# Kernel optimization log

Measured on AMD Instinct MI355X. Metric: run time of the kernel, lower is better.

## Reference

```python
import jax, jax.numpy as jnp
import numpy as np

DIM, D_STATE, D_CONV = 1024, 16, 4
B, T = 2, 4096


def setup_inputs() -> dict:
    key = jax.random.key(0)
    ks = jax.random.split(key, 10)
    s = 0.02
    x = jax.random.normal(ks[0], (B, T, DIM), dtype=jnp.float32)
    W_in = jax.random.normal(ks[1], (DIM, 2 * DIM), dtype=jnp.float32) * s
    conv_w = jax.random.normal(ks[2], (DIM, D_CONV), dtype=jnp.float32) * s
    conv_b = jnp.zeros((DIM,), dtype=jnp.float32)
    A_log = jnp.log(jnp.tile(jnp.arange(1, D_STATE + 1, dtype=jnp.float32), (DIM, 1)))
    D_param = jnp.ones((DIM,), dtype=jnp.float32)
    W_x = jax.random.normal(ks[3], (DIM, 2 * D_STATE), dtype=jnp.float32) * s
    W_dt = jax.random.normal(ks[4], (DIM, DIM), dtype=jnp.float32) * s
    b_dt = jnp.zeros((DIM,), dtype=jnp.float32)
    W_out = jax.random.normal(ks[5], (DIM, DIM), dtype=jnp.float32) * s
    return {"x": x, "W_in": W_in, "conv_w": conv_w, "conv_b": conv_b,
            "A_log": A_log, "D_param": D_param, "W_x": W_x,
            "W_dt": W_dt, "b_dt": b_dt, "W_out": W_out}


def _mamba_fwd(x, W_in, conv_w, conv_b, A_log, D_param, W_x, W_dt, b_dt, W_out):
    Bsz, Tlen, D = x.shape
    N = A_log.shape[1]
    # input projection and gate split
    xz = jnp.einsum('btd,de->bte', x, W_in)          # [B,T,2D]
    x_in, z = jnp.split(xz, 2, axis=-1)
    # causal depthwise conv1d (torch pads both sides d_conv-1 then slices [:T] == left-pad only)
    xc = jnp.transpose(x_in, (0, 2, 1))               # [B,D,T]
    kern = conv_w[:, None, :]                         # [D,1,K] (O,I/groups,K)
    xc = jax.lax.conv_general_dilated(
        xc, kern, window_strides=(1,), padding=[(D_CONV - 1, 0)],
        dimension_numbers=('NCH', 'OIH', 'NCH'), feature_group_count=D)
    xc = xc + conv_b[None, :, None]
    x_in = jnp.transpose(xc, (0, 2, 1))               # [B,T,D]
    x_in = jax.nn.silu(x_in)
    # SSM parameters
    A = -jnp.exp(A_log)                               # [D,N]
    BC = jnp.einsum('btd,dn->btn', x_in, W_x)         # [B,T,2N]
    Bm, Cm = jnp.split(BC, 2, axis=-1)                # each [B,T,N]
    dt = jax.nn.softplus(jnp.einsum('btd,de->bte', x_in, W_dt) + b_dt)  # [B,T,D]
    # selective scan over time
    def step(h, inputs):
        dt_t, B_t, C_t, x_t = inputs                  # [B,D],[B,N],[B,N],[B,D]
        A_eff = jnp.exp(dt_t[:, :, None] * A[None])   # [B,D,N]
        B_eff = dt_t[:, :, None] * B_t[:, None, :]    # [B,D,N]
        h = A_eff * h + B_eff * x_t[:, :, None]
        y_t = jnp.sum(h * C_t[:, None, :], axis=-1) + D_param * x_t
        return h, y_t
    h0 = jnp.zeros((Bsz, D, N), dtype=x.dtype)
    xs = (jnp.transpose(dt, (1, 0, 2)), jnp.transpose(Bm, (1, 0, 2)),
          jnp.transpose(Cm, (1, 0, 2)), jnp.transpose(x_in, (1, 0, 2)))
    _, ys = jax.lax.scan(step, h0, xs)                # ys: [T,B,D]
    y = jnp.transpose(ys, (1, 0, 2))                  # [B,T,D]
    y = y * jax.nn.silu(z)
    return jnp.einsum('btd,de->bte', y, W_out)


def reference(x, W_in, conv_w, conv_b, A_log, D_param, W_x, W_dt, b_dt, W_out):
    return _mamba_fwd(x, W_in, conv_w, conv_b, A_log, D_param, W_x, W_dt, b_dt, W_out)
```

## Files before the change

### kernel.cpp

```cpp
#include <hip/hip_runtime.h>
#include <math.h>

#define DIM 1024
#define DSTATE 16
#define DCONV 4
#define BATCH 2
#define TLEN 4096
#define NC 128
#define LC (TLEN / NC)

typedef short s16x8 __attribute__((ext_vector_type(8)));
typedef float f32x4 __attribute__((ext_vector_type(4)));

__device__ __forceinline__ unsigned short f32_to_bf16(float f) {
    unsigned int u = __float_as_uint(f);
    u += 0x7fffu + ((u >> 16) & 1u);
    return (unsigned short)(u >> 16);
}
__device__ __forceinline__ float bf16_to_f32(unsigned short s) {
    return __uint_as_float(((unsigned int)s) << 16);
}

__device__ __forceinline__ void async16(const void* g, void* l) {
    __builtin_amdgcn_global_load_lds(
        (const __attribute__((address_space(1))) void*)g,
        (__attribute__((address_space(3))) void*)l, 16, 0, 0);
}

__device__ __forceinline__ size_t ps_addr(size_t i) {
    return ((i >> 10) << 11) | (i & 1023);
}

template <int EPI>
__global__ __launch_bounds__(256) void gemm_bf16s(
    const unsigned short* __restrict__ Ah, const unsigned short* __restrict__ Al,
    const unsigned short* __restrict__ Bh, const unsigned short* __restrict__ Bl,
    const float* __restrict__ bias, float* __restrict__ C,
    float* __restrict__ C2, int M, int N, int K)
{
    __shared__ unsigned short sAh[128][32];
    __shared__ unsigned short sAl[128][32];
    __shared__ unsigned short sBh[128][32];
    __shared__ unsigned short sBl[128][32];

    const int tid  = threadIdx.x;
    const int lane = tid & 63;
    const int w    = tid >> 6;
    const int wm   = (w >> 1) * 64;
    const int wn   = (w & 1) * 64;
    const int m0   = blockIdx.y * 128;
    const int n0   = blockIdx.x * 128;

    f32x4 acc[4][4];
#pragma unroll
    for (int i = 0; i < 4; ++i)
#pragma unroll
        for (int j = 0; j < 4; ++j) acc[i][j] = (f32x4){0.f, 0.f, 0.f, 0.f};

    const int srow  = w * 16 + (lane >> 2);
    const int skoff = (((lane & 3) ^ ((lane >> 3) & 3)) * 8);
    const size_t aRow0 = (size_t)(m0 + srow) * K;
    const size_t aRow1 = (size_t)(m0 + srow + 64) * K;
    const size_t bRow0 = (size_t)(n0 + srow) * K;
    const size_t bRow1 = (size_t)(n0 + srow + 64) * K;

    const int frow = lane & 15;
    const int fqd  = (((lane >> 4) ^ ((lane >> 1) & 3)) * 8);

    for (int k0 = 0; k0 < K; k0 += 32) {
        __syncthreads();
        async16(&Ah[aRow0 + k0 + skoff], &sAh[w * 16][0]);
        async16(&Ah[aRow1 + k0 + skoff], &sAh[64 + w * 16][0]);
        async16(&Al[aRow0 + k0 + skoff], &sAl[w * 16][0]);
        async16(&Al[aRow1 + k0 + skoff], &sAl[64 + w * 16][0]);
        async16(&Bh[bRow0 + k0 + skoff], &sBh[w * 16][0]);
        async16(&Bh[bRow1 + k0 + skoff], &sBh[64 + w * 16][0]);
        async16(&Bl[bRow0 + k0 + skoff], &sBl[w * 16][0]);
        async16(&Bl[bRow1 + k0 + skoff], &sBl[64 + w * 16][0]);
        __syncthreads();

        s16x8 fah[4], fal[4], fbh[4], fbl[4];
#pragma unroll
        for (int i = 0; i < 4; ++i) {
            fah[i] = *(const s16x8*)&sAh[wm + i * 16 + frow][fqd];
            fal[i] = *(const s16x8*)&sAl[wm + i * 16 + frow][fqd];
            fbh[i] = *(const s16x8*)&sBh[wn + i * 16 + frow][fqd];
            fbl[i] = *(const s16x8*)&sBl[wn + i * 16 + frow][fqd];
        }
#pragma unroll
        for (int mi = 0; mi < 4; ++mi)
#pragma unroll
            for (int ni = 0; ni < 4; ++ni) {
                acc[mi][ni] = __builtin_amdgcn_mfma_f32_16x16x32_bf16(
                    fah[mi], fbh[ni], acc[mi][ni], 0, 0, 0);
                acc[mi][ni] = __builtin_amdgcn_mfma_f32_16x16x32_bf16(
                    fah[mi], fbl[ni], acc[mi][ni], 0, 0, 0);
                acc[mi][ni] = __builtin_amdgcn_mfma_f32_16x16x32_bf16(
                    fal[mi], fbh[ni], acc[mi][ni], 0, 0, 0);
            }
    }

    const int erow = (lane >> 4) * 4;
    const int ecol = lane & 15;
#pragma unroll
    for (int mi = 0; mi < 4; ++mi)
#pragma unroll
        for (int ni = 0; ni < 4; ++ni) {
            const int colbase = n0 + wn + ni * 16;
            if (EPI == 2 && colbase >= 1024 + 2 * DSTATE) continue;
            const int col = colbase + ecol;
            if (EPI == 2 && colbase >= 1024) {
#pragma unroll
                for (int r = 0; r < 4; ++r) {
                    const int row = m0 + wm + mi * 16 + erow + r;
                    C2[(size_t)row * (2 * DSTATE) + (col - 1024)] = acc[mi][ni][r];
                }
            } else {
                const float bv = (EPI >= 1) ? bias[col] : 0.f;
                const int ldc = (EPI == 2) ? DIM : N;
#pragma unroll
                for (int r = 0; r < 4; ++r) {
                    const int row = m0 + wm + mi * 16 + erow + r;
                    float v = acc[mi][ni][r];
                    if (EPI >= 1) {
                        v += bv;
                        v = (v > 20.f) ? v : log1pf(__expf(v));
                    }
                    C[(size_t)row * ldc + col] = v;
                }
            }
        }
}

__global__ __launch_bounds__(256) void split_kernel(
    const float* __restrict__ src, unsigned short* __restrict__ h,
    unsigned short* __restrict__ l)
{
    size_t i = (size_t)blockIdx.x * 256 + threadIdx.x;
    float v = src[i];
    unsigned short hv = f32_to_bf16(v);
    h[i] = hv;
    l[i] = f32_to_bf16(v - bf16_to_f32(hv));
}

__global__ __launch_bounds__(256) void split_transpose_kernel(
    const float* __restrict__ W, unsigned short* __restrict__ Th,
    unsigned short* __restrict__ Tl, int Kdim, int Ndim)
{
    __shared__ float tile[32][33];
    const int n0 = blockIdx.x * 32;
    const int k0 = blockIdx.y * 32;
    const int tx = threadIdx.x & 31;
    const int ty = threadIdx.x >> 5;
    for (int r = ty; r < 32; r += 8)
        tile[r][tx] = W[(size_t)(k0 + r) * Ndim + n0 + tx];
    __syncthreads();
    for (int r = ty; r < 32; r += 8) {
        float v = tile[tx][r];
        unsigned short hv = f32_to_bf16(v);
        size_t o = (size_t)(n0 + r) * Kdim + k0 + tx;
        Th[o] = hv;
        Tl[o] = f32_to_bf16(v - bf16_to_f32(hv));
    }
}

__global__ __launch_bounds__(256) void conv_silu_kernel(
    const float* __restrict__ xz, const float* __restrict__ conv_w,
    const float* __restrict__ conv_b, float* __restrict__ x_in,
    unsigned short* __restrict__ xh, unsigned short* __restrict__ xl)
{
    size_t idx = (size_t)blockIdx.x * 256 + threadIdx.x;
    int d = (int)(idx & (DIM - 1));
    size_t bt = idx >> 10;
    int t = (int)(bt & (TLEN - 1));

    float acc = conv_b[d];
#pragma unroll
    for (int k = 0; k < DCONV; ++k) {
        int tt = t - (DCONV - 1) + k;
        if (tt >= 0) {
            acc = fmaf(xz[(bt - (DCONV - 1) + k) * (2 * DIM) + d],
                       conv_w[d * DCONV + k], acc);
        }
    }
    float s = acc / (1.f + __expf(-acc));
    x_in[idx] = s;
    unsigned short hv = f32_to_bf16(s);
    xh[idx] = hv;
    xl[idx] = f32_to_bf16(s - bf16_to_f32(hv));
}

__global__ __launch_bounds__(256) void scan_pass_a(
    const float* __restrict__ dt, const float* __restrict__ BC,
    const float* __restrict__ x_in, const float* __restrict__ A_log,
    float* __restrict__ Pb, float* __restrict__ Sb)
{
    __shared__ float sB[LC][DSTATE];
    const int tid = threadIdx.x;
    int blk = blockIdx.x;
    const int dt4 = blk & 3;  blk >>= 2;
    const int c = blk & (NC - 1); blk >>= 7;
    const int b = blk;
    const int d = dt4 * 256 + tid;
    const size_t base = (size_t)b * TLEN + (size_t)c * LC;

    if (tid < LC * DSTATE / 4) {
        const int row = tid >> 2, c4 = tid & 3;
        *(f32x4*)&sB[row][c4 * 4] =
            *(const f32x4*)&BC[(base + row) * (2 * DSTATE) + c4 * 4];
    }

    float A[DSTATE];
#pragma unroll
    for (int q = 0; q < 4; ++q) {
        f32x4 v = *(const f32x4*)&A_log[(size_t)d * DSTATE + q * 4];
        A[q * 4 + 0] = -__expf(v.x); A[q * 4 + 1] = -__expf(v.y);
        A[q * 4 + 2] = -__expf(v.z); A[q * 4 + 3] = -__expf(v.w);
    }
    __syncthreads();

    float h[DSTATE];
#pragma unroll
    for (int n = 0; n < DSTATE; ++n) h[n] = 0.f;
    float sdt = 0.f;

    for (int t = 0; t < LC; ++t) {
        const float dtv = dt[(base + t) * DIM + d];
        const float xv  = x_in[(base + t) * DIM + d];
        sdt += dtv;
        const float dbx = dtv * xv;
#pragma unroll
        for (int n = 0; n < DSTATE; ++n) {
            const float a = __expf(dtv * A[n]);
            h[n] = fmaf(a, h[n], dbx * sB[t][n]);
        }
    }

    const size_t po = ps_addr((((size_t)c * BATCH + b) * DIM + d) * DSTATE);
#pragma unroll
    for (int q = 0; q < 4; ++q) {
        f32x4 pv;
        pv.x = __expf(A[q * 4 + 0] * sdt);
        pv.y = __expf(A[q * 4 + 1] * sdt);
        pv.z = __expf(A[q * 4 + 2] * sdt);
        pv.w = __expf(A[q * 4 + 3] * sdt);
        *(f32x4*)&Pb[po + q * 4] = pv;
        *(f32x4*)&Sb[po + q * 4] = *(f32x4*)&h[q * 4];
    }
}

__global__ __launch_bounds__(256) void scan_pass_b(
    float* __restrict__ Pb, const float* __restrict__ Sb)
{
    const size_t idx = (size_t)blockIdx.x * 256 + threadIdx.x;
    float h = 0.f;
#pragma unroll 4
    for (int c = 0; c < NC; ++c) {
        const size_t o = (size_t)c * (BATCH * DIM * DSTATE) + idx;
        const size_t a = ps_addr(o);
        const float p = Pb[a];
        const float s = Sb[a];
        Pb[a] = h;
        h = fmaf(p, h, s);
    }
}

__global__ __launch_bounds__(256) void scan_pass_c(
    const float* __restrict__ dt, const float* __restrict__ BC,
    const float* __restrict__ xz, const float* __restrict__ A_log,
    const float* __restrict__ D_param, const float* __restrict__ Hin,
    const float* __restrict__ x_in,
    unsigned short* __restrict__ yh, unsigned short* __restrict__ yl)
{
    __shared__ float sB[LC][DSTATE];
    __shared__ float sC[LC][DSTATE];
    const int tid = threadIdx.x;
    int blk = blockIdx.x;
    const int dt4 = blk & 3;  blk >>= 2;
    const int c = blk & (NC - 1); blk >>= 7;
    const int b = blk;
    const int d = dt4 * 256 + tid;
    const size_t base = (size_t)b * TLEN + (size_t)c * LC;

    if (tid < 128) {
        const int row = tid >> 2, c4 = tid & 3;
        *(f32x4*)&sB[row][c4 * 4] =
            *(const f32x4*)&BC[(base + row) * (2 * DSTATE) + c4 * 4];
    } else {
        const int sj = tid - 128;
        const int row = sj >> 2, c4 = sj & 3;
        *(f32x4*)&sC[row][c4 * 4] =
            *(const f32x4*)&BC[(base + row) * (2 * DSTATE) + DSTATE + c4 * 4];
    }

    float A[DSTATE];
#pragma unroll
    for (int q = 0; q < 4; ++q) {
        f32x4 v = *(const f32x4*)&A_log[(size_t)d * DSTATE + q * 4];
        A[q * 4 + 0] = -__expf(v.x); A[q * 4 + 1] = -__expf(v.y);
        A[q * 4 + 2] = -__expf(v.z); A[q * 4 + 3] = -__expf(v.w);
    }
    const float Dp = D_param[d];

    float h[DSTATE];
    const size_t po = ps_addr((((size_t)c * BATCH + b) * DIM + d) * DSTATE);
#pragma unroll
    for (int q = 0; q < 4; ++q)
        *(f32x4*)&h[q * 4] = *(const f32x4*)&Hin[po + q * 4];
    __syncthreads();

    for (int t = 0; t < LC; ++t) {
        const float dtv = dt[(base + t) * DIM + d];
        const float xv  = x_in[(base + t) * DIM + d];
        const float zv  = xz[(base + t) * (2 * DIM) + DIM + d];
        const float dbx = dtv * xv;
        float y0 = 0.f, y1 = 0.f, y2 = 0.f, y3 = 0.f;
#pragma unroll
        for (int q = 0; q < 4; ++q) {
            float a0 = __expf(dtv * A[q * 4 + 0]);
            float a1 = __expf(dtv * A[q * 4 + 1]);
            float a2 = __expf(dtv * A[q * 4 + 2]);
            float a3 = __expf(dtv * A[q * 4 + 3]);
            h[q * 4 + 0] = fmaf(a0, h[q * 4 + 0], dbx * sB[t][q * 4 + 0]);
            h[q * 4 + 1] = fmaf(a1, h[q * 4 + 1], dbx * sB[t][q * 4 + 1]);
            h[q * 4 + 2] = fmaf(a2, h[q * 4 + 2], dbx * sB[t][q * 4 + 2]);
            h[q * 4 + 3] = fmaf(a3, h[q * 4 + 3], dbx * sB[t][q * 4 + 3]);
            y0 = fmaf(h[q * 4 + 0], sC[t][q * 4 + 0], y0);
            y1 = fmaf(h[q * 4 + 1], sC[t][q * 4 + 1], y1);
            y2 = fmaf(h[q * 4 + 2], sC[t][q * 4 + 2], y2);
            y3 = fmaf(h[q * 4 + 3], sC[t][q * 4 + 3], y3);
        }
        float y = (y0 + y1) + (y2 + y3) + Dp * xv;
        const float sig = 1.f / (1.f + __expf(-zv));
        const float yg = y * (zv * sig);
        unsigned short hv = f32_to_bf16(yg);
        yh[(base + t) * DIM + d] = hv;
        yl[(base + t) * DIM + d] = f32_to_bf16(yg - bf16_to_f32(hv));
    }
}

extern "C" void kernel_launch(void* const* d_in, const int* in_sizes, int n_in,
                              void* d_out, int out_size, void* d_ws, size_t ws_size,
                              hipStream_t stream)
{
    const float* x      = (const float*)d_in[0];
    const float* W_in   = (const float*)d_in[1];
    const float* conv_w = (const float*)d_in[2];
    const float* conv_b = (const float*)d_in[3];
    const float* A_log  = (const float*)d_in[4];
    const float* D_par  = (const float*)d_in[5];
    const float* W_x    = (const float*)d_in[6];
    const float* W_dt   = (const float*)d_in[7];
    const float* b_dt   = (const float*)d_in[8];
    const float* W_out  = (const float*)d_in[9];
    float* out = (float*)d_out;

    const size_t BT = (size_t)BATCH * TLEN;
    float* ws = (float*)d_ws;
    float* xz   = ws;
    float* x_in = xz + BT * (2 * DIM);
    float* dtb  = x_in + BT * DIM;
    float* BCb  = dtb + BT * DIM;

    unsigned short* bfAh = (unsigned short*)(BCb + BT * 2 * DSTATE);
    unsigned short* bfAl = bfAh + BT * DIM;
    unsigned short* WinTh = bfAl + BT * DIM;
    unsigned short* WinTl = WinTh + (size_t)2048 * 1024;
    unsigned short* W2Th  = WinTl + (size_t)2048 * 1024;
    unsigned short* W2Tl  = W2Th + (size_t)1152 * 1024;
    unsigned short* WoutTh = W2Tl + (size_t)1152 * 1024;
    unsigned short* WoutTl = WoutTh + (size_t)1024 * 1024;

    float* Pb = xz;
    float* Sb = xz + (size_t)4096 * 2048;

    split_kernel<<<(int)(BT * DIM / 256), 256, 0, stream>>>(x, bfAh, bfAl);
    split_transpose_kernel<<<dim3(2048 / 32, 1024 / 32), 256, 0, stream>>>(
        W_in, WinTh, WinTl, 1024, 2048);
    split_transpose_kernel<<<dim3(1024 / 32, 1024 / 32), 256, 0, stream>>>(
        W_dt, W2Th, W2Tl, 1024, 1024);
    split_transpose_kernel<<<dim3(1, 1024 / 32), 256, 0, stream>>>(
        W_x, W2Th + (size_t)1024 * 1024, W2Tl + (size_t)1024 * 1024, 1024, 32);
    split_transpose_kernel<<<dim3(1024 / 32, 1024 / 32), 256, 0, stream>>>(
        W_out, WoutTh, WoutTl, 1024, 1024);

    gemm_bf16s<0><<<dim3(2048 / 128, BT / 128), 256, 0, stream>>>(
        bfAh, bfAl, WinTh, WinTl, nullptr, xz, nullptr, (int)BT, 2 * DIM, DIM);

    conv_silu_kernel<<<(int)(BT * DIM / 256), 256, 0, stream>>>(
        xz, conv_w, conv_b, x_in, bfAh, bfAl);

    gemm_bf16s<2><<<dim3(1152 / 128, BT / 128), 256, 0, stream>>>(
        bfAh, bfAl, W2Th, W2Tl, b_dt, dtb, BCb, (int)BT, 1152, DIM);

    {
        int grid_ac = BATCH * NC * (DIM / 256);
        scan_pass_a<<<grid_ac, 256, 0, stream>>>(dtb, BCb, x_in, A_log, Pb, Sb);
        scan_pass_b<<<(BATCH * DIM * DSTATE) / 256, 256, 0, stream>>>(Pb, Sb);
        scan_pass_c<<<grid_ac, 256, 0, stream>>>(dtb, BCb, xz, A_log, D_par, Pb,
                                                 x_in, bfAh, bfAl);
    }

    gemm_bf16s<0><<<dim3(1024 / 128, BT / 128), 256, 0, stream>>>(
        bfAh, bfAl, WoutTh, WoutTl, nullptr, out, nullptr, (int)BT, DIM, DIM);
}
```

Before: 549.6 us.

## Use 32x32 MFMA in GEMM, fuse prep kernels, vectorize conv

The split-bf16 GEMM now uses 32x32x16 MFMA tiles with 2x2 accumulators per wave instead of 4x4 16x16x32 tiles. This cuts LDS fragment reads per MFMA and issues fewer, larger instructions. The five separate split and transpose launches are merged into one prep kernel with a vectorized x split, and conv_silu processes four channels per thread using vector loads and stores. The risks are an incorrect output-row mapping for the 32x32 layout and more register pressure from the larger accumulators.

Measured after the change: 523.0 us. 1.05x faster.

```diff
diff --git a/kernel.cpp b/kernel.cpp
--- a/kernel.cpp
+++ b/kernel.cpp
@@ -9,8 +9,10 @@
 #define NC 128
 #define LC (TLEN / NC)
 
+typedef short s16x4 __attribute__((ext_vector_type(4)));
 typedef short s16x8 __attribute__((ext_vector_type(8)));
 typedef float f32x4 __attribute__((ext_vector_type(4)));
+typedef float f32x16 __attribute__((ext_vector_type(16)));
 
 __device__ __forceinline__ unsigned short f32_to_bf16(float f) {
     unsigned int u = __float_as_uint(f);
@@ -51,11 +53,13 @@
     const int m0   = blockIdx.y * 128;
     const int n0   = blockIdx.x * 128;
 
-    f32x4 acc[4][4];
-#pragma unroll
-    for (int i = 0; i < 4; ++i)
-#pragma unroll
-        for (int j = 0; j < 4; ++j) acc[i][j] = (f32x4){0.f, 0.f, 0.f, 0.f};
+    f32x16 acc[2][2];
+#pragma unroll
+    for (int i = 0; i < 2; ++i)
+#pragma unroll
+        for (int j = 0; j < 2; ++j)
+#pragma unroll
+            for (int r = 0; r < 16; ++r) acc[i][j][r] = 0.f;
 
     const int srow  = w * 16 + (lane >> 2);
     const int skoff = (((lane & 3) ^ ((lane >> 3) & 3)) * 8);
@@ -64,8 +68,9 @@
     const size_t bRow0 = (size_t)(n0 + srow) * K;
     const size_t bRow1 = (size_t)(n0 + srow + 64) * K;
 
-    const int frow = lane & 15;
-    const int fqd  = (((lane >> 4) ^ ((lane >> 1) & 3)) * 8);
+    const int frow = lane & 31;
+    const int fkh  = lane >> 5;
+    const int fsw  = (lane >> 1) & 3;
 
     for (int k0 = 0; k0 < K; k0 += 32) {
         __syncthreads();
@@ -79,49 +84,53 @@
         async16(&Bl[bRow1 + k0 + skoff], &sBl[64 + w * 16][0]);
         __syncthreads();
 
-        s16x8 fah[4], fal[4], fbh[4], fbl[4];
-#pragma unroll
-        for (int i = 0; i < 4; ++i) {
-            fah[i] = *(const s16x8*)&sAh[wm + i * 16 + frow][fqd];
-            fal[i] = *(const s16x8*)&sAl[wm + i * 16 + frow][fqd];
-            fbh[i] = *(const s16x8*)&sBh[wn + i * 16 + frow][fqd];
-            fbl[i] = *(const s16x8*)&sBl[wn + i * 16 + frow][fqd];
-        }
-#pragma unroll
-        for (int mi = 0; mi < 4; ++mi)
-#pragma unroll
-            for (int ni = 0; ni < 4; ++ni) {
-                acc[mi][ni] = __builtin_amdgcn_mfma_f32_16x16x32_bf16(
-                    fah[mi], fbh[ni], acc[mi][ni], 0, 0, 0);
-                acc[mi][ni] = __builtin_amdgcn_mfma_f32_16x16x32_bf16(
-                    fah[mi], fbl[ni], acc[mi][ni], 0, 0, 0);
-                acc[mi][ni] = __builtin_amdgcn_mfma_f32_16x16x32_bf16(
-                    fal[mi], fbh[ni], acc[mi][ni], 0, 0, 0);
+#pragma unroll
+        for (int ks = 0; ks < 2; ++ks) {
+            const int pc = (((ks << 1) | fkh) ^ fsw) << 3;
+            s16x8 fah[2], fal[2], fbh[2], fbl[2];
+#pragma unroll
+            for (int i = 0; i < 2; ++i) {
+                fah[i] = *(const s16x8*)&sAh[wm + i * 32 + frow][pc];
+                fal[i] = *(const s16x8*)&sAl[wm + i * 32 + frow][pc];
+                fbh[i] = *(const s16x8*)&sBh[wn + i * 32 + frow][pc];
+                fbl[i] = *(const s16x8*)&sBl[wn + i * 32 + frow][pc];
             }
-    }
-
-    const int erow = (lane >> 4) * 4;
-    const int ecol = lane & 15;
-#pragma unroll
-    for (int mi = 0; mi < 4; ++mi)
-#pragma unroll
-        for (int ni = 0; ni < 4; ++ni) {
-            const int colbase = n0 + wn + ni * 16;
+#pragma unroll
+            for (int mt = 0; mt < 2; ++mt)
+#pragma unroll
+                for (int nt = 0; nt < 2; ++nt) {
+                    acc[mt][nt] = __builtin_amdgcn_mfma_f32_32x32x16_bf16(
+                        fah[mt], fbh[nt], acc[mt][nt], 0, 0, 0);
+                    acc[mt][nt] = __builtin_amdgcn_mfma_f32_32x32x16_bf16(
+                        fah[mt], fbl[nt], acc[mt][nt], 0, 0, 0);
+                    acc[mt][nt] = __builtin_amdgcn_mfma_f32_32x32x16_bf16(
+                        fal[mt], fbh[nt], acc[mt][nt], 0, 0, 0);
+                }
+        }
+    }
+
+    const int ecol  = lane & 31;
+    const int erow4 = (lane >> 5) * 4;
+#pragma unroll
+    for (int mt = 0; mt < 2; ++mt)
+#pragma unroll
+        for (int nt = 0; nt < 2; ++nt) {
+            const int colbase = n0 + wn + nt * 32;
             if (EPI == 2 && colbase >= 1024 + 2 * DSTATE) continue;
             const int col = colbase + ecol;
             if (EPI == 2 && colbase >= 1024) {
 #pragma unroll
-                for (int r = 0; r < 4; ++r) {
-                    const int row = m0 + wm + mi * 16 + erow + r;
-                    C2[(size_t)row * (2 * DSTATE) + (col - 1024)] = acc[mi][ni][r];
+                for (int r = 0; r < 16; ++r) {
+                    const int row = m0 + wm + mt * 32 + (r & 3) + 8 * (r >> 2) + erow4;
+                    C2[(size_t)row * (2 * DSTATE) + (col - 1024)] = acc[mt][nt][r];
                 }
             } else {
                 const float bv = (EPI >= 1) ? bias[col] : 0.f;
                 const int ldc = (EPI == 2) ? DIM : N;
 #pragma unroll
-                for (int r = 0; r < 4; ++r) {
-                    const int row = m0 + wm + mi * 16 + erow + r;
-                    float v = acc[mi][ni][r];
+                for (int r = 0; r < 16; ++r) {
+                    const int row = m0 + wm + mt * 32 + (r & 3) + 8 * (r >> 2) + erow4;
+                    float v = acc[mt][nt][r];
                     if (EPI >= 1) {
                         v += bv;
                         v = (v > 20.f) ? v : log1pf(__expf(v));
@@ -132,26 +141,15 @@
         }
 }
 
-__global__ __launch_bounds__(256) void split_kernel(
-    const float* __restrict__ src, unsigned short* __restrict__ h,
-    unsigned short* __restrict__ l)
-{
-    size_t i = (size_t)blockIdx.x * 256 + threadIdx.x;
-    float v = src[i];
-    unsigned short hv = f32_to_bf16(v);
-    h[i] = hv;
-    l[i] = f32_to_bf16(v - bf16_to_f32(hv));
-}
-
-__global__ __launch_bounds__(256) void split_transpose_kernel(
+__device__ __forceinline__ void tsplit(
     const float* __restrict__ W, unsigned short* __restrict__ Th,
-    unsigned short* __restrict__ Tl, int Kdim, int Ndim)
-{
-    __shared__ float tile[32][33];
-    const int n0 = blockIdx.x * 32;
-    const int k0 = blockIdx.y * 32;
-    const int tx = threadIdx.x & 31;
-    const int ty = threadIdx.x >> 5;
+    unsigned short* __restrict__ Tl, int Kdim, int Ndim, int bx, int by,
+    int tid, float (*tile)[33])
+{
+    const int n0 = bx * 32;
+    const int k0 = by * 32;
+    const int tx = tid & 31;
+    const int ty = tid >> 5;
     for (int r = ty; r < 32; r += 8)
         tile[r][tx] = W[(size_t)(k0 + r) * Ndim + n0 + tx];
     __syncthreads();
@@ -164,30 +162,82 @@
     }
 }
 
+__global__ __launch_bounds__(256) void prep_kernel(
+    const float* __restrict__ x, const float* __restrict__ W_in,
+    const float* __restrict__ W_dt, const float* __restrict__ W_x,
+    const float* __restrict__ W_out,
+    unsigned short* __restrict__ xh, unsigned short* __restrict__ xl,
+    unsigned short* __restrict__ WinTh, unsigned short* __restrict__ WinTl,
+    unsigned short* __restrict__ W2Th, unsigned short* __restrict__ W2Tl,
+    unsigned short* __restrict__ WoutTh, unsigned short* __restrict__ WoutTl)
+{
+    __shared__ float tile[32][33];
+    const int tid = threadIdx.x;
+    const int blk = blockIdx.x;
+    if (blk < 2048) {
+        tsplit(W_in, WinTh, WinTl, 1024, 2048, blk & 63, blk >> 6, tid, tile);
+    } else if (blk < 3072) {
+        const int b2 = blk - 2048;
+        tsplit(W_dt, W2Th, W2Tl, 1024, 1024, b2 & 31, b2 >> 5, tid, tile);
+    } else if (blk < 3104) {
+        tsplit(W_x, W2Th + (size_t)1024 * 1024, W2Tl + (size_t)1024 * 1024,
+               1024, 32, 0, blk - 3072, tid, tile);
+    } else if (blk < 4128) {
+        const int b2 = blk - 3104;
+        tsplit(W_out, WoutTh, WoutTl, 1024, 1024, b2 & 31, b2 >> 5, tid, tile);
+    } else {
+        const size_t i = ((size_t)(blk - 4128) * 256 + tid) * 4;
+        f32x4 v = *(const f32x4*)&x[i];
+        s16x4 h, l;
+#pragma unroll
+        for (int j = 0; j < 4; ++j) {
+            unsigned short hv = f32_to_bf16(v[j]);
+            h[j] = (short)hv;
+            l[j] = (short)f32_to_bf16(v[j] - bf16_to_f32(hv));
+        }
+        *(s16x4*)&xh[i] = h;
+        *(s16x4*)&xl[i] = l;
+    }
+}
+
 __global__ __launch_bounds__(256) void conv_silu_kernel(
     const float* __restrict__ xz, const float* __restrict__ conv_w,
     const float* __restrict__ conv_b, float* __restrict__ x_in,
     unsigned short* __restrict__ xh, unsigned short* __restrict__ xl)
 {
-    size_t idx = (size_t)blockIdx.x * 256 + threadIdx.x;
-    int d = (int)(idx & (DIM - 1));
-    size_t bt = idx >> 10;
-    int t = (int)(bt & (TLEN - 1));
-
-    float acc = conv_b[d];
+    const size_t idx4 = ((size_t)blockIdx.x * 256 + threadIdx.x) * 4;
+    const int d = (int)(idx4 & (DIM - 1));
+    const size_t bt = idx4 >> 10;
+    const int t = (int)(bt & (TLEN - 1));
+
+    f32x4 acc = *(const f32x4*)&conv_b[d];
+    f32x4 w0 = *(const f32x4*)&conv_w[(d + 0) * DCONV];
+    f32x4 w1 = *(const f32x4*)&conv_w[(d + 1) * DCONV];
+    f32x4 w2 = *(const f32x4*)&conv_w[(d + 2) * DCONV];
+    f32x4 w3 = *(const f32x4*)&conv_w[(d + 3) * DCONV];
 #pragma unroll
     for (int k = 0; k < DCONV; ++k) {
-        int tt = t - (DCONV - 1) + k;
+        const int tt = t - (DCONV - 1) + k;
         if (tt >= 0) {
-            acc = fmaf(xz[(bt - (DCONV - 1) + k) * (2 * DIM) + d],
-                       conv_w[d * DCONV + k], acc);
-        }
-    }
-    float s = acc / (1.f + __expf(-acc));
-    x_in[idx] = s;
-    unsigned short hv = f32_to_bf16(s);
-    xh[idx] = hv;
-    xl[idx] = f32_to_bf16(s - bf16_to_f32(hv));
+            f32x4 xv = *(const f32x4*)&xz[(bt - (DCONV - 1) + k) * (2 * DIM) + d];
+            acc.x = fmaf(xv.x, w0[k], acc.x);
+            acc.y = fmaf(xv.y, w1[k], acc.y);
+            acc.z = fmaf(xv.z, w2[k], acc.z);
+            acc.w = fmaf(xv.w, w3[k], acc.w);
+        }
+    }
+    f32x4 s;
+    s16x4 h, l;
+#pragma unroll
+    for (int j = 0; j < 4; ++j) {
+        s[j] = acc[j] / (1.f + __expf(-acc[j]));
+        unsigned short hv = f32_to_bf16(s[j]);
+        h[j] = (short)hv;
+        l[j] = (short)f32_to_bf16(s[j] - bf16_to_f32(hv));
+    }
+    *(f32x4*)&x_in[idx4] = s;
+    *(s16x4*)&xh[idx4] = h;
+    *(s16x4*)&xl[idx4] = l;
 }
 
 __global__ __launch_bounds__(256) void scan_pass_a(
@@ -374,20 +424,14 @@
     float* Pb = xz;
     float* Sb = xz + (size_t)4096 * 2048;
 
-    split_kernel<<<(int)(BT * DIM / 256), 256, 0, stream>>>(x, bfAh, bfAl);
-    split_transpose_kernel<<<dim3(2048 / 32, 1024 / 32), 256, 0, stream>>>(
-        W_in, WinTh, WinTl, 1024, 2048);
-    split_transpose_kernel<<<dim3(1024 / 32, 1024 / 32), 256, 0, stream>>>(
-        W_dt, W2Th, W2Tl, 1024, 1024);
-    split_transpose_kernel<<<dim3(1, 1024 / 32), 256, 0, stream>>>(
-        W_x, W2Th + (size_t)1024 * 1024, W2Tl + (size_t)1024 * 1024, 1024, 32);
-    split_transpose_kernel<<<dim3(1024 / 32, 1024 / 32), 256, 0, stream>>>(
-        W_out, WoutTh, WoutTl, 1024, 1024);
+    prep_kernel<<<12320, 256, 0, stream>>>(
+        x, W_in, W_dt, W_x, W_out, bfAh, bfAl,
+        WinTh, WinTl, W2Th, W2Tl, WoutTh, WoutTl);
 
     gemm_bf16s<0><<<dim3(2048 / 128, BT / 128), 256, 0, stream>>>(
         bfAh, bfAl, WinTh, WinTl, nullptr, xz, nullptr, (int)BT, 2 * DIM, DIM);
 
-    conv_silu_kernel<<<(int)(BT * DIM / 256), 256, 0, stream>>>(
+    conv_silu_kernel<<<(int)(BT * DIM / 1024), 256, 0, stream>>>(
         xz, conv_w, conv_b, x_in, bfAh, bfAl);
 
     gemm_bf16s<2><<<dim3(1152 / 128, BT / 128), 256, 0, stream>>>(
```
